# Kernel optimization log

Measured on AMD Instinct MI355X. Metric: run time of the kernel, lower is better.

## Reference

```python
import jax, jax.numpy as jnp
import numpy as np

INPUT_DIM, ENC_H, DEC_H, HORIZON = 8, 384, 384, 18
B, L = 1024, 336


def _lstm_layer(xs, Wih, Whh, bih, bhh):
    # xs: [B, L, D] -> outputs [B, L, H], final h [B, H]
    Bv = xs.shape[0]
    Hh = Whh.shape[1]
    def step(carry, x_t):
        h, c = carry
        z = x_t @ Wih.T + h @ Whh.T + bih + bhh  # [B, 4H], gate order i,f,g,o (PyTorch)
        i, f, g, o = jnp.split(z, 4, axis=-1)
        c = jax.nn.sigmoid(f) * c + jax.nn.sigmoid(i) * jnp.tanh(g)
        h = jax.nn.sigmoid(o) * jnp.tanh(c)
        return (h, c), h
    init = (jnp.zeros((Bv, Hh), xs.dtype), jnp.zeros((Bv, Hh), xs.dtype))
    (h, c), ys = jax.lax.scan(step, init, jnp.swapaxes(xs, 0, 1))
    return jnp.swapaxes(ys, 0, 1), h


def setup_inputs() -> dict:
    key = jax.random.key(0)
    ks = jax.random.split(key, 20)
    s = 0.05
    d = {
        "x": jax.random.normal(ks[0], (B, L, INPUT_DIM), jnp.float32),
        "future_feats": jax.random.normal(ks[1], (B, HORIZON, 4), jnp.float32),
        # encoder layer 0
        "enc_Wih0": jax.random.normal(ks[2], (4 * ENC_H, INPUT_DIM), jnp.float32) * s,
        "enc_Whh0": jax.random.normal(ks[3], (4 * ENC_H, ENC_H), jnp.float32) * s,
        "enc_bih0": jax.random.normal(ks[4], (4 * ENC_H,), jnp.float32) * s,
        "enc_bhh0": jax.random.normal(ks[5], (4 * ENC_H,), jnp.float32) * s,
        # encoder layer 1
        "enc_Wih1": jax.random.normal(ks[6], (4 * ENC_H, ENC_H), jnp.float32) * s,
        "enc_Whh1": jax.random.normal(ks[7], (4 * ENC_H, ENC_H), jnp.float32) * s,
        "enc_bih1": jax.random.normal(ks[8], (4 * ENC_H,), jnp.float32) * s,
        "enc_bhh1": jax.random.normal(ks[9], (4 * ENC_H,), jnp.float32) * s,
        # attention projection (no bias)
        "Wa": jax.random.normal(ks[10], (DEC_H, ENC_H), jnp.float32) * s,
        # dec_in: Linear(1+4+enc_h -> dec_h)
        "dec_in_W": jax.random.normal(ks[11], (DEC_H, 1 + 4 + ENC_H), jnp.float32) * s,
        "dec_in_b": jax.random.normal(ks[12], (DEC_H,), jnp.float32) * s,
        # decoder LSTM (1 layer)
        "dec_Wih": jax.random.normal(ks[13], (4 * DEC_H, DEC_H), jnp.float32) * s,
        "dec_Whh": jax.random.normal(ks[14], (4 * DEC_H, DEC_H), jnp.float32) * s,
        "dec_bih": jax.random.normal(ks[15], (4 * DEC_H,), jnp.float32) * s,
        "dec_bhh": jax.random.normal(ks[16], (4 * DEC_H,), jnp.float32) * s,
        # output head
        "out_W": jax.random.normal(ks[17], (1, DEC_H), jnp.float32) * s,
        "out_b": jax.random.normal(ks[18], (1,), jnp.float32) * s,
    }
    return d


def reference(x, future_feats, enc_Wih0, enc_Whh0, enc_bih0, enc_bhh0,
              enc_Wih1, enc_Whh1, enc_bih1, enc_bhh1, Wa, dec_in_W, dec_in_b,
              dec_Wih, dec_Whh, dec_bih, dec_bhh, out_W, out_b):
    Bv = x.shape[0]
    # 2-layer encoder (eval mode: inter-layer dropout inactive)
    h1, _ = _lstm_layer(x, enc_Wih0, enc_Whh0, enc_bih0, enc_bhh0)
    enc_out, h_last = _lstm_layer(h1, enc_Wih1, enc_Whh1, enc_bih1, enc_bhh1)
    proj = enc_out @ Wa.T  # [B, L, dec_h] (Wa(enc_out) is step-invariant)

    def dec_step(carry, feat_t):
        h, c, y_prev = carry
        scores = jnp.einsum('bld,bd->bl', proj, h)
        alpha = jax.nn.softmax(scores, axis=1)
        ctx = jnp.einsum('bl,bld->bd', alpha, enc_out)
        din = jnp.concatenate([y_prev, feat_t, ctx], axis=1)  # [B, 1+4+enc_h]
        din = jax.nn.relu(din @ dec_in_W.T + dec_in_b)
        z = din @ dec_Wih.T + h @ dec_Whh.T + dec_bih + dec_bhh
        i, f, g, o = jnp.split(z, 4, axis=-1)
        c = jax.nn.sigmoid(f) * c + jax.nn.sigmoid(i) * jnp.tanh(g)
        h = jax.nn.sigmoid(o) * jnp.tanh(c)
        y_t = h @ out_W.T + out_b  # [B, 1]
        y_prev = jax.lax.stop_gradient(y_t)  # .detach() in torch
        return (h, c, y_prev), y_t

    init = (h_last, jnp.zeros_like(h_last), jnp.zeros((Bv, 1), x.dtype))
    _, ys = jax.lax.scan(dec_step, init, jnp.swapaxes(future_feats, 0, 1))
    return jnp.swapaxes(ys, 0, 1)  # [B, horizon, 1]
```

## Files before the change

kernel.cpp:

```cpp
#include <hip/hip_runtime.h>
#include <stdint.h>

typedef __bf16 bf16;
typedef __bf16 bf16x8 __attribute__((ext_vector_type(8)));
typedef short  s16x8  __attribute__((ext_vector_type(8)));
typedef float  f32x4  __attribute__((ext_vector_type(4)));
typedef uint32_t u32;

#define NB   1024
#define LSEQ 336
#define HID  384
#define HOR  18
#define SMEM_BYTES 36864
#define E1T  ((size_t)24*NB*16)

__device__ bf16  g_H0[(size_t)(LSEQ+1)*NB*HID];
__device__ bf16  g_E1[(size_t)(LSEQ+1)*E1T];
__device__ bf16  g_enc[(size_t)NB*LSEQ*HID];
__device__ bf16  g_Adec[2*NB*768];
__device__ bf16  g_Adin[NB*416];
__device__ bf16  g_xb[NB*LSEQ*8];
__device__ float g_cdec[NB*HID];
__device__ float g_u[NB*HID];
__device__ float g_bias0[1536], g_bias1[1536], g_biasd[1536], g_biasdin[384];
__device__ bf16  g_Bp0[12*13*4096];
__device__ bf16  g_Bp1n[24*24*4*64*8];
__device__ bf16  g_Bpd[12*24*4096];
__device__ bf16  g_Bpi[3*13*4096];
__device__ bf16  g_Bpu[3*12*4096];
__device__ int   g_f0[8*LSEQ];
__device__ int   g_f1[4*(LSEQ+1)];

__device__ __forceinline__ float sigf(float x){ return 1.0f/(1.0f + __expf(-x)); }
__device__ __forceinline__ float tanh_f(float x){
  x = fminf(fmaxf(x, -15.f), 15.f);
  float e = __expf(2.f*x);
  return (e - 1.f)/(e + 1.f);
}

__global__ void zero_state_k(){
  int i = blockIdx.x*blockDim.x + threadIdx.x;
  int st = gridDim.x*blockDim.x;
  bf16 z = (bf16)0.f;
  for(int k=i;k<NB*HID;k+=st){ g_H0[k]=z; g_E1[k]=z; g_cdec[k]=0.f; }
  for(int k=i;k<8*LSEQ;k+=st) g_f0[k]=0;
  for(int k=i;k<4*(LSEQ+1);k+=st) g_f1[k]=0;
}

__global__ void pack_xb_k(const float* __restrict__ x){
  int i = blockIdx.x*256 + threadIdx.x;
  int n = NB*LSEQ*8;
  for(int k=i; k<n; k+=gridDim.x*256) g_xb[k] = (bf16)x[k];
}

__global__ void pack_gates_k(int mode, const float* __restrict__ W1, const float* __restrict__ W2,
                             int nks){
  bf16* out = (mode==0)? g_Bp0 : g_Bpd;
  size_t idx = (size_t)blockIdx.x*256 + threadIdx.x;
  size_t total = (size_t)12*nks*512;
  if(idx >= total) return;
  int lane = (int)(idx & 63);
  int tt   = (int)((idx>>6) & 7);
  size_t tmp = idx >> 9;
  int ks = (int)(tmp % nks);
  int jb = (int)(tmp / nks);
  int n  = (tt>>1)*HID + jb*32 + (tt&1)*16 + (lane&15);
  int kb = ks*32 + (lane>>4)*8;
  bf16x8 v;
  #pragma unroll
  for(int i=0;i<8;i++){
    int k = kb + i;
    float f;
    if(mode==0) f = (k<384) ? W1[(size_t)n*384 + k] : (k<392 ? W2[(size_t)n*8 + (k-384)] : 0.f);
    else        f = (k<384) ? W1[(size_t)n*384 + k] : W2[(size_t)n*384 + (k-384)];
    v[i] = (bf16)f;
  }
  *(bf16x8*)(out + idx*8) = v;
}

__global__ void pack_gates16_k(const float* __restrict__ Wih1, const float* __restrict__ Whh1){
  int idx = blockIdx.x*256 + threadIdx.x;
  if(idx >= 24*24*4*64) return;
  int lane = idx&63, rem = idx>>6;
  int g = rem&3; rem >>= 2;
  int ks = rem%24, jn = rem/24;
  int n  = g*HID + jn*16 + (lane&15);
  int kb = ks*32 + (lane>>4)*8;
  bf16x8 v;
  #pragma unroll
  for(int i=0;i<8;i++){
    int k = kb+i;
    float f = (k<384)? Wih1[(size_t)n*384 + k] : Whh1[(size_t)n*384 + (k-384)];
    v[i] = (bf16)f;
  }
  *(bf16x8*)(g_Bp1n + (size_t)idx*8) = v;
}

__global__ void pack_plain_k(int mode, const float* __restrict__ W, int nks, int nb_cnt){
  bf16* out = mode ? g_Bpu : g_Bpi;
  size_t idx = (size_t)blockIdx.x*256 + threadIdx.x;
  size_t total = (size_t)nb_cnt*nks*512;
  if(idx>=total) return;
  int lane = (int)(idx&63);
  int tt   = (int)((idx>>6)&7);
  size_t tmp = idx>>9;
  int ks = (int)(tmp%nks);
  int nb = (int)(tmp/nks);
  int n  = nb*128 + tt*16 + (lane&15);
  int kb = ks*32 + (lane>>4)*8;
  bf16x8 v;
  #pragma unroll
  for(int i=0;i<8;i++){
    int k = kb+i;
    float f;
    if(mode==0) f = (k<389)? W[(size_t)n*389 + k] : 0.f;
    else        f = W[(size_t)k*384 + n];
    v[i]=(bf16)f;
  }
  *(bf16x8*)(out + idx*8) = v;
}

__global__ void prep_misc_k(const float* bih0,const float* bhh0,const float* bih1,const float* bhh1,
                            const float* dbih,const float* dbhh,const float* dinb){
  int i = blockIdx.x*256 + threadIdx.x;
  if(i<1536){ g_bias0[i]=bih0[i]+bhh0[i]; g_bias1[i]=bih1[i]+bhh1[i]; g_biasd[i]=dbih[i]+dbhh[i]; }
  if(i<384) g_biasdin[i]=dinb[i];
}

__device__ __forceinline__ void spin_ge(int* p, int tgt){
  while(__hip_atomic_load(p, __ATOMIC_RELAXED, __HIP_MEMORY_SCOPE_AGENT) < tgt){}
}
__device__ __forceinline__ void release_agent(){
  __builtin_amdgcn_fence(__ATOMIC_RELEASE, "agent");
}

__global__ __launch_bounds__(256,1)
void enc8_k(){
  extern __shared__ char lds[];
  const int bid = blockIdx.x, tid = threadIdx.x;
  const int lane = tid&63, wv = tid>>6;
  const int l15 = lane&15, lk = (lane>>4)*8;

  if(bid < 96){
    const int g = bid & 7, jb = bid >> 3;
    { const s16x8* src = (const s16x8*)(g_Bp0 + (size_t)jb*13*4096);
      s16x8* dst = (s16x8*)lds;
      #pragma unroll
      for(int h=0;h<26;h++) dst[tid + h*256] = src[tid + h*256];
    }
    bf16* tr = (bf16*)(lds + 13*8192);
    __syncthreads();
    const int jj0 = jb*32 + l15;
    float bia[2],bfa[2],bga[2],boa[2];
    #pragma unroll
    for(int jh=0;jh<2;jh++){
      bia[jh]=g_bias0[jj0+jh*16];     bfa[jh]=g_bias0[384+jj0+jh*16];
      bga[jh]=g_bias0[768+jj0+jh*16]; boa[jh]=g_bias0[1152+jj0+jh*16];
    }
    size_t hoff[2], xoff[2];
    #pragma unroll
    for(int mt=0;mt<2;mt++){
      int row = g*128 + wv*32 + mt*16 + l15;
      hoff[mt] = (size_t)row*HID + lk;
      xoff[mt] = (size_t)row*LSEQ*8;
    }
    float c[2][2][4] = {};
    for(int w=0; w<LSEQ; w++){
      if(tid==0 && w>=1) spin_ge(&g_f0[g*LSEQ + (w-1)], 12);
      __syncthreads();
      asm volatile("" ::: "memory");
      const bf16* H0w = g_H0 + (size_t)w*NB*HID;
      bf16x8 af[13][2];
      #pragma unroll
      for(int ks=0;ks<12;ks++)
        #pragma unroll
        for(int mt=0;mt<2;mt++)
          af[ks][mt] = *(const bf16x8*)(H0w + hoff[mt] + ks*32);
      #pragma unroll
      for(int mt=0;mt<2;mt++){
        bf16x8 z;
        #pragma unroll
        for(int e=0;e<8;e++) z[e]=(bf16)0.f;
        if(lk==0) z = *(const bf16x8*)(g_xb + xoff[mt] + (size_t)w*8);
        af[12][mt] = z;
      }
      f32x4 acc[2][8];
      #pragma unroll
      for(int m2=0;m2<2;m2++)
        #pragma unroll
        for(int tt=0;tt<8;tt++) acc[m2][tt] = (f32x4){0.f,0.f,0.f,0.f};
      #pragma unroll
      for(int ks=0;ks<13;ks++){
        #pragma unroll
        for(int tt=0;tt<8;tt++){
          bf16x8 bfr = *(const bf16x8*)(lds + (ks*8+tt)*1024 + lane*16);
          acc[0][tt] = __builtin_amdgcn_mfma_f32_16x16x32_bf16(af[ks][0], bfr, acc[0][tt],0,0,0);
          acc[1][tt] = __builtin_amdgcn_mfma_f32_16x16x32_bf16(af[ks][1], bfr, acc[1][tt],0,0,0);
        }
      }
      #pragma unroll
      for(int mt=0;mt<2;mt++)
        #pragma unroll
        for(int jh=0;jh<2;jh++)
          #pragma unroll
          for(int r=0;r<4;r++){
            float zi=acc[mt][0+jh][r]+bia[jh], zf=acc[mt][2+jh][r]+bfa[jh],
                  zg=acc[mt][4+jh][r]+bga[jh], zo=acc[mt][6+jh][r]+boa[jh];
            float cn = sigf(zf)*c[mt][jh][r] + sigf(zi)*tanh_f(zg);
            c[mt][jh][r]=cn;
            int lr = wv*32 + mt*16 + (lane>>4)*4 + r;
            tr[lr*32 + jh*16 + l15] = (bf16)(sigf(zo)*tanh_f(cn));
          }
      __syncthreads();
      bf16* H0n = g_H0 + (size_t)(w+1)*NB*HID;
      #pragma unroll
      for(int h=0;h<2;h++){
        int p = tid + h*256;
        int row = p>>2, cc = p&3;
        s16x8 v = *(const s16x8*)(tr + row*32 + cc*8);
        *(s16x8*)(H0n + (size_t)(g*128+row)*HID + jb*32 + cc*8) = v;
      }
      __syncthreads();
      if(tid==0){
        release_agent();
        __hip_atomic_fetch_add(&g_f0[g*LSEQ + w], 1, __ATOMIC_RELAXED, __HIP_MEMORY_SCOPE_AGENT);
      }
    }
  } else {
    const int idx = bid-96, m = idx & 3, jn = idx >> 2;
    { const s16x8* src = (const s16x8*)(g_Bp1n + (size_t)jn*24*2048);
      s16x8* dst = (s16x8*)lds;
      #pragma unroll
      for(int h=0;h<24;h++) dst[tid + h*256] = src[tid + h*256];
    }
    bf16* tr = (bf16*)(lds + 24*4096);
    __syncthreads();
    const int jj = jn*16 + l15;
    const float bi=g_bias1[jj], bff=g_bias1[384+jj], bg=g_bias1[768+jj], bo=g_bias1[1152+jj];
    int rows[4]; size_t hoff[4], eo[4];
    const int jn_half = (lane>>4)>>1, colin = ((lane>>4)&1)*8;
    #pragma unroll
    for(int mt=0;mt<4;mt++){
      rows[mt] = m*256 + wv*64 + mt*16 + l15;
      hoff[mt] = (size_t)rows[mt]*HID + lk;
      eo[mt]   = (size_t)jn_half*(NB*16) + (size_t)rows[mt]*16 + colin;
    }
    float c[4][4] = {};
    for(int s=1; s<=LSEQ; s++){
      if(tid==0)      spin_ge(&g_f0[(2*m)*LSEQ + (s-1)], 12);
      else if(tid==1) spin_ge(&g_f0[(2*m+1)*LSEQ + (s-1)], 12);
      __syncthreads();
      asm volatile("" ::: "memory");
      const bf16* H0s = g_H0 + (size_t)s*NB*HID;
      const bf16* Es  = g_E1 + (size_t)(s-1)*E1T;
      bf16x8 ap[8][4];
      #pragma unroll
      for(int d=0; d<8; d++)
        #pragma unroll
        for(int mt=0;mt<4;mt++)
          ap[d][mt] = *(const bf16x8*)(H0s + hoff[mt] + d*32);
      if(tid==0 && s>=2) spin_ge(&g_f1[m*(LSEQ+1) + (s-1)], 24);
      __syncthreads();
      asm volatile("" ::: "memory");
      f32x4 acc[4][4];
      #pragma unroll
      for(int mt=0;mt<4;mt++)
        #pragma unroll
        for(int g4=0;g4<4;g4++) acc[mt][g4] = (f32x4){0.f,0.f,0.f,0.f};
      #pragma unroll
      for(int ks=0;ks<24;ks++){
        bf16x8 bfr[4];
        #pragma unroll
        for(int g4=0;g4<4;g4++) bfr[g4] = *(const bf16x8*)(lds + (ks*4+g4)*1024 + lane*16);
        bf16x8 a[4];
        #pragma unroll
        for(int mt=0;mt<4;mt++) a[mt] = ap[ks&7][mt];
        int kn = ks+8;
        if(kn<24){
          if(kn<12){
            #pragma unroll
            for(int mt=0;mt<4;mt++) ap[ks&7][mt] = *(const bf16x8*)(H0s + hoff[mt] + kn*32);
          } else {
            #pragma unroll
            for(int mt=0;mt<4;mt++) ap[ks&7][mt] = *(const bf16x8*)(Es + (size_t)(kn-12)*32768 + eo[mt]);
          }
        }
        #pragma unroll
        for(int mt=0;mt<4;mt++)
          #pragma unroll
          for(int g4=0;g4<4;g4++)
            acc[mt][g4] = __builtin_amdgcn_mfma_f32_16x16x32_bf16(a[mt], bfr[g4], acc[mt][g4],0,0,0);
      }
      #pragma unroll
      for(int mt=0;mt<4;mt++)
        #pragma unroll
        for(int r=0;r<4;r++){
          float zi=acc[mt][0][r]+bi, zf=acc[mt][1][r]+bff,
                zg=acc[mt][2][r]+bg, zo=acc[mt][3][r]+bo;
          float cn = sigf(zf)*c[mt][r] + sigf(zi)*tanh_f(zg);
          c[mt][r]=cn;
          int lr = wv*64 + mt*16 + (lane>>4)*4 + r;
          tr[lr*16 + l15] = (bf16)(sigf(zo)*tanh_f(cn));
        }
      __syncthreads();
      bf16* E1w = g_E1 + (size_t)s*E1T + (size_t)jn*(NB*16);
      #pragma unroll
      for(int h=0;h<2;h++){
        int p = tid + h*256;
        int row = p>>1, hf2 = p&1;
        s16x8 v = *(const s16x8*)(tr + row*16 + hf2*8);
        *(s16x8*)(E1w + (size_t)(m*256+row)*16 + hf2*8) = v;
      }
      if((jn&1)==0 && s>=2){
        const int t_out = s-2;
        const bf16* Ep = g_E1 + (size_t)(s-1)*E1T;
        #pragma unroll
        for(int h=0;h<4;h++){
          int cch = tid + h*256;
          int row = cch>>2, seg = cch&3;
          const bf16* srcp = Ep + (size_t)(jn + (seg>>1))*(NB*16) + (size_t)(m*256+row)*16 + (seg&1)*8;
          s16x8 v = *(const s16x8*)srcp;
          *(s16x8*)(g_enc + ((size_t)(m*256+row)*LSEQ + t_out)*HID + jn*16 + seg*8) = v;
        }
      }
      __syncthreads();
      if(tid==0){
        release_agent();
        __hip_atomic_fetch_add(&g_f1[m*(LSEQ+1) + s], 1, __ATOMIC_RELAXED, __HIP_MEMORY_SCOPE_AGENT);
      }
    }
    if(tid==0) spin_ge(&g_f1[m*(LSEQ+1) + LSEQ], 24);
    __syncthreads();
    asm volatile("" ::: "memory");
    if((jn&1)==0){
      const bf16* Ep = g_E1 + (size_t)LSEQ*E1T;
      #pragma unroll
      for(int h=0;h<4;h++){
        int cch = tid + h*256;
        int row = cch>>2, seg = cch&3;
        const bf16* srcp = Ep + (size_t)(jn + (seg>>1))*(NB*16) + (size_t)(m*256+row)*16 + (seg&1)*8;
        s16x8 v = *(const s16x8*)srcp;
        *(s16x8*)(g_enc + ((size_t)(m*256+row)*LSEQ + (LSEQ-1))*HID + jn*16 + seg*8) = v;
      }
    }
  }
}

struct SReg { s16x8 a0,a1,b0,b1; };

__device__ __forceinline__ void stage_load(const bf16* __restrict__ A, int ldA,
                                           const bf16* __restrict__ Bk, int tid, SReg& sr){
  int c0 = tid, c1 = tid+256;
  sr.a0 = *(const s16x8*)(A + (size_t)(c0>>2)*ldA + (c0&3)*8);
  sr.a1 = *(const s16x8*)(A + (size_t)(c1>>2)*ldA + (c1&3)*8);
  const s16x8* B8 = (const s16x8*)Bk;
  sr.b0 = B8[c0]; sr.b1 = B8[c1];
}

__device__ __forceinline__ void stage_write(char* Ab, char* Bb, int tid, const SReg& sr){
  int c0 = tid, c1 = tid+256;
  *(s16x8*)(Ab + (c0>>2)*80 + (c0&3)*16) = sr.a0;
  *(s16x8*)(Ab + (c1>>2)*80 + (c1&3)*16) = sr.a1;
  *(s16x8*)(Bb + c0*16) = sr.b0;
  *(s16x8*)(Bb + c1*16) = sr.b1;
}

__device__ __forceinline__ void gemm_core(const bf16* __restrict__ A, int ldA,
                                          const bf16* __restrict__ Bp, int nks,
                                          char* smem, f32x4 acc[4][4]){
  const int tid = threadIdx.x;
  const int lane = tid & 63, wv = tid>>6, wm = wv>>1, wn = wv&1;
  char* Ab0 = smem;            char* Ab1 = smem + 10240;
  char* Bb0 = smem + 20480;    char* Bb1 = smem + 28672;
  f32x4 z = {0.f,0.f,0.f,0.f};
  #pragma unroll
  for(int m=0;m<4;m++)
    #pragma unroll
    for(int g=0;g<4;g++) acc[m][g]=z;
  SReg sr;
  stage_load(A, ldA, Bp, tid, sr);
  stage_write(Ab0, Bb0, tid, sr);
  const int aoff = (wm*64 + (lane&15))*80 + (lane>>4)*16;
  const int boff = wn*1024 + lane*16;
  for(int ks=0; ks<nks; ks++){
    char* Ac = (ks&1)? Ab1: Ab0;
    char* Bc = (ks&1)? Bb1: Bb0;
    char* An = (ks&1)? Ab0: Ab1;
    char* Bn = (ks&1)? Bb0: Bb1;
    bool more = (ks+1)<nks;
    if(more) stage_load(A + (ks+1)*32, ldA, Bp + (size_t)(ks+1)*4096, tid, sr);
    __syncthreads();
    bf16x8 af[4], bfr[4];
    #pragma unroll
    for(int mt=0;mt<4;mt++) af[mt] = *(const bf16x8*)(Ac + aoff + mt*16*80);
    #pragma unroll
    for(int g=0;g<4;g++)    bfr[g] = *(const bf16x8*)(Bc + boff + g*2048);
    #pragma unroll
    for(int mt=0;mt<4;mt++)
      #pragma unroll
      for(int g=0;g<4;g++)
        acc[mt][g] = __builtin_amdgcn_mfma_f32_16x16x32_bf16(af[mt], bfr[g], acc[mt][g], 0,0,0);
    if(more) stage_write(An, Bn, tid, sr);
  }
}

__device__ __forceinline__ void lstm_epi(f32x4 acc[4][4], int mbase, int jb,
     const float* __restrict__ bias, float* __restrict__ cst,
     bf16* __restrict__ d0, int ld0, bf16* __restrict__ d1, size_t ld1){
  int lane = threadIdx.x&63, wv = threadIdx.x>>6, wm = wv>>1, wn = wv&1;
  int j = jb*32 + wn*16 + (lane&15);
  float bi = bias[j], bff = bias[384+j], bg = bias[768+j], bo = bias[1152+j];
  #pragma unroll
  for(int mt=0;mt<4;mt++){
    #pragma unroll
    for(int r=0;r<4;r++){
      int brow = mbase + wm*64 + mt*16 + (lane>>4)*4 + r;
      float zi = acc[mt][0][r]+bi, zf = acc[mt][1][r]+bff,
            zg = acc[mt][2][r]+bg, zo = acc[mt][3][r]+bo;
      size_t ci = (size_t)brow*HID + j;
      float cold = cst[ci];
      float cn = sigf(zf)*cold + sigf(zi)*tanh_f(zg);
      cst[ci] = cn;
      bf16 hb = (bf16)(sigf(zo)*tanh_f(cn));
      d0[(size_t)brow*ld0 + j] = hb;
      if(d1) d1[(size_t)brow*ld1 + j] = hb;
    }
  }
}

__global__ __launch_bounds__(256)
void dec_lstm_k(int t){
  __shared__ char smem[SMEM_BYTES];
  int bid = blockIdx.x, mb = bid/12, jb = bid%12;
  int rs = t&1, wsl = rs^1;
  f32x4 acc[4][4];
  gemm_core(g_Adec + (size_t)rs*NB*768 + (size_t)mb*128*768, 768,
            g_Bpd + (size_t)jb*24*4096, 24, smem, acc);
  lstm_epi(acc, mb*128, jb, g_biasd, g_cdec,
           g_Adec + (size_t)wsl*NB*768 + 384, 768, (bf16*)nullptr, 0);
}

__global__ __launch_bounds__(256)
void plain_gemm_k(int t, int mode, const float* __restrict__ outW,
                  const float* __restrict__ outb, float* __restrict__ out,
                  const float* __restrict__ ff){
  __shared__ char smem[SMEM_BYTES];
  int bid = blockIdx.x, mb = bid/3, nb = bid%3;
  int rs = t&1;
  const bf16* A; int ldA, nks; const bf16* Bp;
  if(mode==1){ A = g_Adec + (size_t)rs*NB*768 + 384; ldA=768; Bp = g_Bpu; nks=12; }
  else       { A = g_Adin;                           ldA=416; Bp = g_Bpi; nks=13; }
  f32x4 acc[4][4];
  gemm_core(A + (size_t)mb*128*ldA, ldA, Bp + (size_t)nb*nks*4096, nks, smem, acc);
  int lane = threadIdx.x&63, wv = threadIdx.x>>6, wm = wv>>1, wn = wv&1;
  bf16* dbf = g_Adec + (size_t)rs*NB*768;
  #pragma unroll
  for(int mt=0;mt<4;mt++){
    #pragma unroll
    for(int ti=0;ti<4;ti++){
      int n = nb*128 + (ti*2+wn)*16 + (lane&15);
      #pragma unroll
      for(int r=0;r<4;r++){
        int brow = mb*128 + wm*64 + mt*16 + (lane>>4)*4 + r;
        float v = acc[mt][ti][r];
        if(mode==0){ v += g_biasdin[n]; v = fmaxf(v,0.f); dbf[(size_t)brow*768 + n] = (bf16)v; }
        else g_u[(size_t)brow*384 + n] = v;
      }
    }
  }
  if(mode==1 && t>=1 && nb==0 && threadIdx.x<128){
    int b = mb*128 + threadIdx.x;
    const s16x8* hp = (const s16x8*)(g_Adec + (size_t)rs*NB*768 + (size_t)b*768 + 384);
    float acc2 = 0.f;
    #pragma unroll 4
    for(int i=0;i<48;i++){
      s16x8 v = hp[i];
      #pragma unroll
      for(int e=0;e<8;e++){
        float hv = __uint_as_float(((u32)(uint16_t)v[e])<<16);
        acc2 += hv*outW[i*8+e];
      }
    }
    float y = acc2 + outb[0];
    out[(size_t)b*HOR + (t-1)] = y;
    g_Adin[(size_t)b*416] = (bf16)y;
    #pragma unroll
    for(int k=0;k<4;k++) g_Adin[(size_t)b*416 + 1 + k] = (bf16)ff[(size_t)b*HOR*4 + t*4 + k];
  }
}

__global__ __launch_bounds__(256)
void attn_k(int t){
  __shared__ float sm[4][392];
  int tid = threadIdx.x, lane = tid&63, w = tid>>6;
  int bl = w>>1, hf = w&1;
  int b = blockIdx.x*2 + bl;
  const float* ub = g_u + (size_t)b*HID + lane*6;
  float u0=ub[0],u1=ub[1],u2=ub[2],u3=ub[3],u4=ub[4],u5=ub[5];
  const u32* er = (const u32*)(g_enc + (size_t)b*LSEQ*HID) + (size_t)hf*168*192 + lane*3;
  int estep = 192;
  if(t & 1){ er += (size_t)167*192; estep = -192; }
  float m=-1e30f, den=0.f, a0=0,a1=0,a2=0,a3=0,a4=0,a5=0;
  for(int l=0;l<168;l++){
    u32 w0 = er[0], w1 = er[1], w2 = er[2];
    er += estep;
    float e0 = __uint_as_float(w0<<16);
    float e1 = __uint_as_float(w0 & 0xffff0000u);
    float e2 = __uint_as_float(w1<<16);
    float e3 = __uint_as_float(w1 & 0xffff0000u);
    float e4 = __uint_as_float(w2<<16);
    float e5 = __uint_as_float(w2 & 0xffff0000u);
    float p = e0*u0 + e1*u1 + e2*u2 + e3*u3 + e4*u4 + e5*u5;
    #pragma unroll
    for(int o=1;o<64;o<<=1) p += __shfl_xor(p, o, 64);
    float mn = fmaxf(m, p);
    float al = __expf(m - mn), pe = __expf(p - mn);
    den = den*al + pe;
    a0 = a0*al + pe*e0; a1 = a1*al + pe*e1; a2 = a2*al + pe*e2;
    a3 = a3*al + pe*e3; a4 = a4*al + pe*e4; a5 = a5*al + pe*e5;
    m = mn;
  }
  if(lane==0){ sm[w][0]=m; sm[w][1]=den; }
  sm[w][2+lane*6+0]=a0; sm[w][2+lane*6+1]=a1; sm[w][2+lane*6+2]=a2;
  sm[w][2+lane*6+3]=a3; sm[w][2+lane*6+4]=a4; sm[w][2+lane*6+5]=a5;
  __syncthreads();
  if(hf==0){
    float m2 = sm[w+1][0], d2 = sm[w+1][1];
    float M = fmaxf(m, m2);
    float f1 = __expf(m - M), f2 = __expf(m2 - M);
    float inv = 1.f/(den*f1 + d2*f2);
    bf16* cd = g_Adin + (size_t)b*416 + 5 + lane*6;
    cd[0] = (bf16)((a0*f1 + sm[w+1][2+lane*6+0]*f2)*inv);
    cd[1] = (bf16)((a1*f1 + sm[w+1][2+lane*6+1]*f2)*inv);
    cd[2] = (bf16)((a2*f1 + sm[w+1][2+lane*6+2]*f2)*inv);
    cd[3] = (bf16)((a3*f1 + sm[w+1][2+lane*6+3]*f2)*inv);
    cd[4] = (bf16)((a4*f1 + sm[w+1][2+lane*6+4]*f2)*inv);
    cd[5] = (bf16)((a5*f1 + sm[w+1][2+lane*6+5]*f2)*inv);
  }
}

__global__ void post_k(int t, const float* __restrict__ outW,
                       const float* __restrict__ outb, float* __restrict__ out){
  int b = blockIdx.x*256 + threadIdx.x;
  if(b>=NB) return;
  int wsl = (t&1)^1;
  const s16x8* hp = (const s16x8*)(g_Adec + (size_t)wsl*NB*768 + (size_t)b*768 + 384);
  float acc = 0.f;
  #pragma unroll 4
  for(int i=0;i<48;i++){
    s16x8 v = hp[i];
    #pragma unroll
    for(int e=0;e<8;e++){
      float hv = __uint_as_float(((u32)(uint16_t)v[e])<<16);
      acc += hv*outW[i*8+e];
    }
  }
  out[(size_t)b*HOR + t] = acc + outb[0];
}

__global__ void dec_prep_k(const float* __restrict__ ff){
  int i = blockIdx.x*256 + threadIdx.x;
  if(i < NB*HID){
    int b = i/HID, j = i%HID;
    g_Adec[(size_t)b*768 + 384 + j] = g_enc[(size_t)b*LSEQ*HID + (size_t)(LSEQ-1)*HID + j];
  }
  if(i < NB*4){
    int b = i>>2, k = i&3;
    g_Adin[(size_t)b*416 + 1 + k] = (bf16)ff[(size_t)b*HOR*4 + k];
  }
  if(i < NB) g_Adin[(size_t)i*416] = (bf16)0.f;
}

extern "C" void kernel_launch(void* const* d_in, const int* in_sizes, int n_in,
                              void* d_out, int out_size, void* d_ws, size_t ws_size,
                              hipStream_t stream){
  const float* x    = (const float*)d_in[0];
  const float* ff   = (const float*)d_in[1];
  const float* Wih0 = (const float*)d_in[2];
  const float* Whh0 = (const float*)d_in[3];
  const float* bih0 = (const float*)d_in[4];
  const float* bhh0 = (const float*)d_in[5];
  const float* Wih1 = (const float*)d_in[6];
  const float* Whh1 = (const float*)d_in[7];
  const float* bih1 = (const float*)d_in[8];
  const float* bhh1 = (const float*)d_in[9];
  const float* Wa   = (const float*)d_in[10];
  const float* dinW = (const float*)d_in[11];
  const float* dinb = (const float*)d_in[12];
  const float* dWih = (const float*)d_in[13];
  const float* dWhh = (const float*)d_in[14];
  const float* dbih = (const float*)d_in[15];
  const float* dbhh = (const float*)d_in[16];
  const float* outW = (const float*)d_in[17];
  const float* outb = (const float*)d_in[18];
  float* out = (float*)d_out;

  zero_state_k<<<1024,256,0,stream>>>();
  pack_xb_k<<<2048,256,0,stream>>>(x);
  pack_gates_k<<<(12*13*512)/256,256,0,stream>>>(0, Whh0, Wih0, 13);
  pack_gates16_k<<<576,256,0,stream>>>(Wih1, Whh1);
  pack_gates_k<<<(12*24*512)/256,256,0,stream>>>(2, dWih, dWhh, 24);
  pack_plain_k<<<(3*13*512)/256,256,0,stream>>>(0, dinW, 13, 3);
  pack_plain_k<<<(3*12*512)/256,256,0,stream>>>(1, Wa, 12, 3);
  prep_misc_k<<<8,256,0,stream>>>(bih0,bhh0,bih1,bhh1,dbih,dbhh,dinb);

  hipFuncSetAttribute((const void*)enc8_k,
                      hipFuncAttributeMaxDynamicSharedMemorySize, 114688);
  enc8_k<<<192,256,114688,stream>>>();

  dec_prep_k<<<1536,256,0,stream>>>(ff);
  for(int t=0;t<HOR;t++){
    plain_gemm_k<<<24,256,0,stream>>>(t, 1, outW, outb, out, ff);
    attn_k<<<512,256,0,stream>>>(t);
    plain_gemm_k<<<24,256,0,stream>>>(t, 0, outW, outb, out, ff);
    dec_lstm_k<<<96,256,0,stream>>>(t);
  }
  post_k<<<4,256,0,stream>>>(17, outW, outb, out);
  (void)in_sizes; (void)n_in; (void)out_size; (void)d_ws; (void)ws_size;
}
```

Baseline: 7.944 ms.

## Replace atomic counter barriers with per-producer padded flags and separate consumer flags

Cross-block step synchronisation in the persistent encoder kernel moves from atomic fetch-add counters polled by one thread to per-producer flags, each padded to its own 64-byte slot. Several threads each poll one flag with s_sleep backoff. Layer-0 producers write two flag copies so layer-1 consumers do not contend with layer-0 peers. The layer-1 flag is now published before the g_enc copy-out rather than after it, and the block-to-(m, jn) mapping is reshuffled. The goal is less contention on atomic cache lines and a shorter critical path per timestep, at the cost of much larger flag arrays to zero and more polling threads.

```diff
diff --git a/kernel.cpp b/kernel.cpp
--- a/kernel.cpp
+++ b/kernel.cpp
@@ -28,8 +28,9 @@
 __device__ bf16  g_Bpd[12*24*4096];
 __device__ bf16  g_Bpi[3*13*4096];
 __device__ bf16  g_Bpu[3*12*4096];
-__device__ int   g_f0[8*LSEQ];
-__device__ int   g_f1[4*(LSEQ+1)];
+__device__ int   g_f0 [8*LSEQ*12*16];
+__device__ int   g_f0m[8*LSEQ*12*16];
+__device__ int   g_f1 [4*(LSEQ+1)*24*16];
 
 __device__ __forceinline__ float sigf(float x){ return 1.0f/(1.0f + __expf(-x)); }
 __device__ __forceinline__ float tanh_f(float x){
@@ -43,8 +44,8 @@
   int st = gridDim.x*blockDim.x;
   bf16 z = (bf16)0.f;
   for(int k=i;k<NB*HID;k+=st){ g_H0[k]=z; g_E1[k]=z; g_cdec[k]=0.f; }
-  for(int k=i;k<8*LSEQ;k+=st) g_f0[k]=0;
-  for(int k=i;k<4*(LSEQ+1);k+=st) g_f1[k]=0;
+  for(int k=i;k<8*LSEQ*12*16;k+=st){ g_f0[k]=0; g_f0m[k]=0; }
+  for(int k=i;k<4*(LSEQ+1)*24*16;k+=st) g_f1[k]=0;
 }
 
 __global__ void pack_xb_k(const float* __restrict__ x){
@@ -127,15 +128,19 @@
   if(i<384) g_biasdin[i]=dinb[i];
 }
 
-__device__ __forceinline__ void spin_ge(int* p, int tgt){
-  while(__hip_atomic_load(p, __ATOMIC_RELAXED, __HIP_MEMORY_SCOPE_AGENT) < tgt){}
+__device__ __forceinline__ void spin_set(int* p){
+  while(__hip_atomic_load(p, __ATOMIC_RELAXED, __HIP_MEMORY_SCOPE_AGENT) == 0)
+    __builtin_amdgcn_s_sleep(2);
+}
+__device__ __forceinline__ void flag_set(int* p){
+  __hip_atomic_store(p, 1, __ATOMIC_RELAXED, __HIP_MEMORY_SCOPE_AGENT);
 }
 __device__ __forceinline__ void release_agent(){
   __builtin_amdgcn_fence(__ATOMIC_RELEASE, "agent");
 }
 
 __global__ __launch_bounds__(256,1)
-void enc8_k(){
+void enc10_k(){
   extern __shared__ char lds[];
   const int bid = blockIdx.x, tid = threadIdx.x;
   const int lane = tid&63, wv = tid>>6;
@@ -166,7 +171,7 @@
     }
     float c[2][2][4] = {};
     for(int w=0; w<LSEQ; w++){
-      if(tid==0 && w>=1) spin_ge(&g_f0[g*LSEQ + (w-1)], 12);
+      if(w>=1 && tid<12) spin_set(&g_f0[((g*LSEQ + (w-1))*12 + tid)*16]);
       __syncthreads();
       asm volatile("" ::: "memory");
       const bf16* H0w = g_H0 + (size_t)w*NB*HID;
@@ -223,11 +228,12 @@
       __syncthreads();
       if(tid==0){
         release_agent();
-        __hip_atomic_fetch_add(&g_f0[g*LSEQ + w], 1, __ATOMIC_RELAXED, __HIP_MEMORY_SCOPE_AGENT);
+        flag_set(&g_f0 [((g*LSEQ + w)*12 + jb)*16]);
+        flag_set(&g_f0m[((g*LSEQ + w)*12 + jb)*16]);
       }
     }
   } else {
-    const int idx = bid-96, m = idx & 3, jn = idx >> 2;
+    const int idx = bid-96, m = (idx&7)>>1, jn = (idx>>3) + (idx&1)*12;
     { const s16x8* src = (const s16x8*)(g_Bp1n + (size_t)jn*24*2048);
       s16x8* dst = (s16x8*)lds;
       #pragma unroll
@@ -247,8 +253,10 @@
     }
     float c[4][4] = {};
     for(int s=1; s<=LSEQ; s++){
-      if(tid==0)      spin_ge(&g_f0[(2*m)*LSEQ + (s-1)], 12);
-      else if(tid==1) spin_ge(&g_f0[(2*m+1)*LSEQ + (s-1)], 12);
+      if(tid<24){
+        int gg = 2*m + (tid>=12);
+        spin_set(&g_f0m[((gg*LSEQ + (s-1))*12 + (tid%12))*16]);
+      }
       __syncthreads();
       asm volatile("" ::: "memory");
       const bf16* H0s = g_H0 + (size_t)s*NB*HID;
@@ -259,7 +267,8 @@
         #pragma unroll
         for(int mt=0;mt<4;mt++)
           ap[d][mt] = *(const bf16x8*)(H0s + hoff[mt] + d*32);
-      if(tid==0 && s>=2) spin_ge(&g_f1[m*(LSEQ+1) + (s-1)], 24);
+      if(s>=2 && tid>=32 && tid<56)
+        spin_set(&g_f1[((m*(LSEQ+1) + (s-1))*24 + (tid-32))*16]);
       __syncthreads();
       asm volatile("" ::: "memory");
       f32x4 acc[4][4];
@@ -311,6 +320,11 @@
         s16x8 v = *(const s16x8*)(tr + row*16 + hf2*8);
         *(s16x8*)(E1w + (size_t)(m*256+row)*16 + hf2*8) = v;
       }
+      __syncthreads();
+      if(tid==0){
+        release_agent();
+        flag_set(&g_f1[((m*(LSEQ+1) + s)*24 + jn)*16]);
+      }
       if((jn&1)==0 && s>=2){
         const int t_out = s-2;
         const bf16* Ep = g_E1 + (size_t)(s-1)*E1T;
@@ -323,13 +337,8 @@
           *(s16x8*)(g_enc + ((size_t)(m*256+row)*LSEQ + t_out)*HID + jn*16 + seg*8) = v;
         }
       }
-      __syncthreads();
-      if(tid==0){
-        release_agent();
-        __hip_atomic_fetch_add(&g_f1[m*(LSEQ+1) + s], 1, __ATOMIC_RELAXED, __HIP_MEMORY_SCOPE_AGENT);
-      }
-    }
-    if(tid==0) spin_ge(&g_f1[m*(LSEQ+1) + LSEQ], 24);
+    }
+    if(tid<24) spin_set(&g_f1[((m*(LSEQ+1) + LSEQ)*24 + tid)*16]);
     __syncthreads();
     asm volatile("" ::: "memory");
     if((jn&1)==0){
@@ -604,9 +613,9 @@
   pack_plain_k<<<(3*12*512)/256,256,0,stream>>>(1, Wa, 12, 3);
   prep_misc_k<<<8,256,0,stream>>>(bih0,bhh0,bih1,bhh1,dbih,dbhh,dinb);
 
-  hipFuncSetAttribute((const void*)enc8_k,
+  hipFuncSetAttribute((const void*)enc10_k,
                       hipFuncAttributeMaxDynamicSharedMemorySize, 114688);
-  enc8_k<<<192,256,114688,stream>>>();
+  enc10_k<<<192,256,114688,stream>>>();
 
   dec_prep_k<<<1536,256,0,stream>>>(ff);
   for(int t=0;t<HOR;t++){
```

After: 7.595 ms. 4.4% less time.
